# Kernel tuning notes

Hardware: AMD Instinct MI355X
Metric: run time of the kernel (lower is better)

Reference implementation:

```python
import jax, jax.numpy as jnp
import numpy as np
from jax import lax

B, TGT, SRC = 2, 1024, 1024
D_MODEL, D_INNER, D_STATE, D_CONV, DT_RANK, D_FF, N_HEADS = 1024, 2048, 16, 4, 64, 4096, 16
EPS = 1e-6


def rmsnorm(x, w):
    return x * lax.rsqrt(jnp.mean(x * x, axis=-1, keepdims=True) + EPS) * w


def weight_quant(w):
    # BitNet b1.58 ternary weight quantization (absmean), straight-through
    s = jnp.clip(jnp.mean(jnp.abs(w)), 1e-5, None)
    wq = jnp.clip(jnp.round(w / s), -1.0, 1.0) * s
    return w + lax.stop_gradient(wq - w)


def act_quant(x):
    # per-token 8-bit absmax activation quantization, straight-through
    s = jnp.clip(jnp.max(jnp.abs(x), axis=-1, keepdims=True), 1e-5, None) / 127.0
    xq = jnp.clip(jnp.round(x / s), -128.0, 127.0) * s
    return x + lax.stop_gradient(xq - x)


def mamba_block(x, in_w, conv_w, conv_b, xproj_w, dt_w, dt_b, A_log, D, out_w):
    # x: (b, L, d_model)
    xz = x @ in_w.T                              # (b, L, 2*d_inner)
    u, res = jnp.split(xz, 2, axis=-1)
    # causal depthwise conv over sequence
    uc = lax.conv_general_dilated(
        u.transpose(0, 2, 1), conv_w, (1,), [(D_CONV - 1, 0)],
        dimension_numbers=('NCH', 'OIH', 'NCH'), feature_group_count=D_INNER)
    u = jax.nn.silu((uc + conv_b[None, :, None]).transpose(0, 2, 1))  # (b, L, d_inner)
    proj = u @ xproj_w.T                         # (b, L, dt_rank + 2*d_state)
    dt, Bm, Cm = jnp.split(proj, [DT_RANK, DT_RANK + D_STATE], axis=-1)
    delta = jax.nn.softplus(dt @ dt_w.T + dt_b)  # (b, L, d_inner)
    A = -jnp.exp(A_log)                          # (d_inner, d_state)
    dA = jnp.exp(delta[..., None] * A)                       # (b, L, d_inner, d_state)
    dBu = (delta * u)[..., None] * Bm[:, :, None, :]         # (b, L, d_inner, d_state)

    def step(h, t):
        da, dbu, c = t
        h = da * h + dbu
        return h, jnp.einsum('bds,bs->bd', h, c)

    h0 = jnp.zeros((x.shape[0], D_INNER, D_STATE), x.dtype)
    _, ys = lax.scan(step, h0, (dA.transpose(1, 0, 2, 3), dBu.transpose(1, 0, 2, 3), Cm.transpose(1, 0, 2)))
    y = ys.transpose(1, 0, 2) + u * D
    return (y * jax.nn.silu(res)) @ out_w.T


def cross_attention(x, enc, mask, qw, qb, kw, kb, vw, vb, ow, ob):
    hd = D_MODEL // N_HEADS
    b, t, _ = x.shape
    s = enc.shape[1]
    q = (x @ qw.T + qb).reshape(b, t, N_HEADS, hd)
    k = (enc @ kw.T + kb).reshape(b, s, N_HEADS, hd)
    v = (enc @ vw.T + vb).reshape(b, s, N_HEADS, hd)
    sc = jnp.einsum('bthd,bshd->bhts', q, k) / np.sqrt(hd)
    sc = jnp.where(mask[:, None, None, :], sc, -1e9)
    a = jax.nn.softmax(sc, axis=-1)
    o = jnp.einsum('bhts,bshd->bthd', a, v).reshape(b, t, D_MODEL)
    return o @ ow.T + ob


def bitnet_ffn(x, w1, b1, w2, b2):
    h = jax.nn.gelu(act_quant(x) @ weight_quant(w1).T + b1)
    return act_quant(h) @ weight_quant(w2).T + b2


def setup_inputs() -> dict:
    key = jax.random.key(0)
    ks = iter(jax.random.split(key, 32))
    n = lambda shape, sc=0.02: (jax.random.normal(next(ks), shape, jnp.float32) * sc)
    inp = {
        'x': jax.random.normal(next(ks), (B, TGT, D_MODEL), jnp.float32),
        'encoder_out': jax.random.normal(next(ks), (B, SRC, D_MODEL), jnp.float32),
        'encoder_mask': jnp.ones((B, SRC), dtype=bool),
        'mamba_in_w': n((2 * D_INNER, D_MODEL)),
        'mamba_conv_w': n((D_INNER, 1, D_CONV), 0.2),
        'mamba_conv_b': jnp.zeros((D_INNER,), jnp.float32),
        'mamba_xproj_w': n((DT_RANK + 2 * D_STATE, D_INNER)),
        'mamba_dt_w': n((D_INNER, DT_RANK)),
        'mamba_dt_b': jnp.full((D_INNER,), -4.0, jnp.float32),
        'mamba_A_log': jnp.broadcast_to(jnp.log(jnp.arange(1, D_STATE + 1, dtype=jnp.float32)), (D_INNER, D_STATE)).copy(),
        'mamba_D': jnp.ones((D_INNER,), jnp.float32),
        'mamba_out_w': n((D_MODEL, D_INNER)),
        'norm1_w': jnp.ones((D_MODEL,), jnp.float32),
        'q_w': n((D_MODEL, D_MODEL)), 'q_b': jnp.zeros((D_MODEL,), jnp.float32),
        'k_w': n((D_MODEL, D_MODEL)), 'k_b': jnp.zeros((D_MODEL,), jnp.float32),
        'v_w': n((D_MODEL, D_MODEL)), 'v_b': jnp.zeros((D_MODEL,), jnp.float32),
        'o_w': n((D_MODEL, D_MODEL)), 'o_b': jnp.zeros((D_MODEL,), jnp.float32),
        'norm2_w': jnp.ones((D_MODEL,), jnp.float32),
        'ffn_w1': n((D_FF, D_MODEL)), 'ffn_b1': jnp.zeros((D_FF,), jnp.float32),
        'ffn_w2': n((D_MODEL, D_FF)), 'ffn_b2': jnp.zeros((D_MODEL,), jnp.float32),
        'norm3_w': jnp.ones((D_MODEL,), jnp.float32),
    }
    return inp


def reference(x, encoder_out, encoder_mask, mamba_in_w, mamba_conv_w, mamba_conv_b,
              mamba_xproj_w, mamba_dt_w, mamba_dt_b, mamba_A_log, mamba_D, mamba_out_w,
              norm1_w, q_w, q_b, k_w, k_b, v_w, v_b, o_w, o_b, norm2_w,
              ffn_w1, ffn_b1, ffn_w2, ffn_b2, norm3_w):
    residual = x
    h = mamba_block(x, mamba_in_w, mamba_conv_w, mamba_conv_b, mamba_xproj_w,
                    mamba_dt_w, mamba_dt_b, mamba_A_log, mamba_D, mamba_out_w)
    h = rmsnorm(residual + h, norm1_w)  # dropout = identity (eval)
    residual = h
    a = cross_attention(h, encoder_out, encoder_mask, q_w, q_b, k_w, k_b, v_w, v_b, o_w, o_b)
    h = rmsnorm(residual + a, norm2_w)
    residual = h
    f = bitnet_ffn(h, ffn_w1, ffn_b1, ffn_w2, ffn_b2)
    return rmsnorm(residual + f, norm3_w)
```

## Files before the change

kernel.cpp:

```cpp
#include <hip/hip_runtime.h>
#include <math.h>

#define DEV __device__ __forceinline__
using u16 = unsigned short;
typedef __bf16 bh8 __attribute__((ext_vector_type(8)));
typedef float f32x4 __attribute__((ext_vector_type(4)));
typedef u16 u16x8 __attribute__((ext_vector_type(8)));
typedef u16 u16x4 __attribute__((ext_vector_type(4)));

DEV float b2f(u16 x){ unsigned u = ((unsigned)x) << 16; float f; __builtin_memcpy(&f, &u, 4); return f; }
DEV u16 f2b(float f){ unsigned u; __builtin_memcpy(&u, &f, 4); return (u16)((u + 0x7fffu + ((u >> 16) & 1u)) >> 16); }
DEV float sigm(float x){ return 1.f / (1.f + __expf(-x)); }
DEV float ldf(const void* p, size_t i, bool f32){ return f32 ? ((const float*)p)[i] : b2f(((const u16*)p)[i]); }

__global__ __launch_bounds__(256) void detect_kernel(const void* x, unsigned* flag)
{
  const int tid = threadIdx.x;
  const u16* p = (const u16*)x;
  int sane = 0;
  #pragma unroll
  for (int j = 0; j < 8; j++){
    u16 v = p[(size_t)(tid * 8 + j) * 2];
    int e = (v >> 7) & 0xFF;
    sane += (e >= 0x60 && e <= 0x8F) ? 1 : 0;
  }
  __shared__ int red[256];
  red[tid] = sane; __syncthreads();
  for (int s = 128; s > 0; s >>= 1){ if (tid < s) red[tid] += red[tid + s]; __syncthreads(); }
  if (tid == 0) flag[0] = (red[0] < 1200) ? 1u : 0u;
}

#define NCVT 17
struct CvtJobs {
  const void* src[NCVT];
  u16* dst[NCVT];
  int n[NCVT];
  int blk_off[NCVT + 1];
};
__global__ __launch_bounds__(256) void convert_kernel(CvtJobs jobs, const unsigned* __restrict__ Fg)
{
  const bool f32 = Fg[0] != 0;
  const int bx = blockIdx.x;
  int j = 0;
  while (bx >= jobs.blk_off[j + 1]) j++;
  const int e = (bx - jobs.blk_off[j]) * 2048 + threadIdx.x * 8;
  if (e >= jobs.n[j]) return;
  if (f32){
    const float* s = (const float*)jobs.src[j] + e;
    u16x8 o;
    #pragma unroll
    for (int i = 0; i < 8; i++) o[i] = f2b(s[i]);
    *(u16x8*)(jobs.dst[j] + e) = o;
  } else {
    *(u16x8*)(jobs.dst[j] + e) = *(const u16x8*)((const u16*)jobs.src[j] + e);
  }
}

template<int EPI, int FM, int FN, int WR, int WC>
__global__ __launch_bounds__(256) void gemm16(
    const u16* __restrict__ A, const u16* __restrict__ W, void* __restrict__ Cv,
    int M, int N, int K, int lda, int ldb, int ldc,
    const u16* __restrict__ bias, const float* __restrict__ rowscale,
    const float* __restrict__ wscale)
{
  constexpr int BM = WR * FM * 16, BN = WC * FN * 16;
  __shared__ __align__(16) char As[BM * 128];
  __shared__ __align__(16) char Bs[BN * 128];
  const int tid = threadIdx.x, wave = tid >> 6, lane = tid & 63;
  const int wr = wave / WC, wc = wave % WC, fr = lane & 15, g = lane >> 4;
  const size_t bm = (size_t)blockIdx.y * BM, bn = (size_t)blockIdx.x * BN;
  const int kbase = blockIdx.z * K;
  f32x4 acc[FM][FN] = {};
  constexpr int ACH = BM / 32, BCH = BN / 32;
  u16x8 areg[ACH], breg[BCH];
  auto fetch = [&](int k0){
    #pragma unroll
    for (int c = 0; c < ACH; c++){
      int li = tid + c * 256;
      areg[c] = *(const u16x8*)&A[(bm + (li >> 3)) * (size_t)lda + kbase + k0 + ((li & 7) << 3)];
    }
    #pragma unroll
    for (int c = 0; c < BCH; c++){
      int li = tid + c * 256;
      breg[c] = *(const u16x8*)&W[(bn + (li >> 3)) * (size_t)ldb + kbase + k0 + ((li & 7) << 3)];
    }
  };
  fetch(0);
  for (int k0 = 0; k0 < K; k0 += 64){
    __syncthreads();
    #pragma unroll
    for (int c = 0; c < ACH; c++){
      int li = tid + c * 256, row = li >> 3, j = li & 7;
      *(u16x8*)&As[row * 128 + ((j * 16) ^ ((row & 7) << 4))] = areg[c];
    }
    #pragma unroll
    for (int c = 0; c < BCH; c++){
      int li = tid + c * 256, row = li >> 3, j = li & 7;
      *(u16x8*)&Bs[row * 128 + ((j * 16) ^ ((row & 7) << 4))] = breg[c];
    }
    __syncthreads();
    if (k0 + 64 < K) fetch(k0 + 64);
    bh8 af[2][FM], bf[2][FN];
    #pragma unroll
    for (int ks = 0; ks < 2; ks++){
      #pragma unroll
      for (int i = 0; i < FM; i++){
        int row = wr * (FM * 16) + i * 16 + fr;
        af[ks][i] = *(const bh8*)&As[row * 128 + ((ks * 64 + g * 16) ^ ((row & 7) << 4))];
      }
      #pragma unroll
      for (int j = 0; j < FN; j++){
        int row = wc * (FN * 16) + j * 16 + fr;
        bf[ks][j] = *(const bh8*)&Bs[row * 128 + ((ks * 64 + g * 16) ^ ((row & 7) << 4))];
      }
    }
    #pragma unroll
    for (int ks = 0; ks < 2; ks++)
      #pragma unroll
      for (int i = 0; i < FM; i++)
        #pragma unroll
        for (int j = 0; j < FN; j++)
          acc[i][j] = __builtin_amdgcn_mfma_f32_16x16x32_bf16(af[ks][i], bf[ks][j], acc[i][j], 0, 0, 0);
  }
  float wsc = 0.f;
  if constexpr (EPI == 4 || EPI == 5) wsc = wscale[0];
  u16* Cb = (u16*)Cv;
  float* Cf = (float*)Cv + (size_t)blockIdx.z * M * ldc;
  #pragma unroll
  for (int i = 0; i < FM; i++){
    #pragma unroll
    for (int r = 0; r < 4; r++){
      const size_t row = bm + wr * (FM * 16) + i * 16 + g * 4 + r;
      float rs = 0.f;
      if constexpr (EPI == 4 || EPI == 5) rs = rowscale[row] * wsc;
      #pragma unroll
      for (int j = 0; j < FN; j++){
        const size_t col = bn + wc * (FN * 16) + j * 16 + fr;
        float v = acc[i][j][r];
        if constexpr (EPI == 1 || EPI == 2) v += b2f(bias[col]);
        if constexpr (EPI == 4 || EPI == 5) v = v * rs + b2f(bias[col]);
        if constexpr (EPI == 4){ float x = v; v = 0.5f * x * (1.f + tanhf(0.7978845608f * (x + 0.044715f * x * x * x))); }
        if constexpr (EPI == 6){ float x = v + b2f(bias[col]); v = fmaxf(x, 0.f) + log1pf(__expf(-fabsf(x))); }
        if constexpr (EPI == 0 || EPI == 1 || EPI == 4) Cb[row * ldc + col] = f2b(v);
        else Cf[row * ldc + col] = v;
      }
    }
  }
}

__global__ __launch_bounds__(256) void xproj_reduce_kernel(
    const float* __restrict__ Pp, float* __restrict__ proj, u16* __restrict__ projb)
{
  const int idx = blockIdx.x * 256 + threadIdx.x;
  const int m = idx / 96, n = idx % 96;
  float s = 0.f;
  #pragma unroll
  for (int z = 0; z < 8; z++) s += Pp[(size_t)z * 2048 * 96 + idx];
  proj[idx] = s;
  if (n < 64) projb[(size_t)m * 64 + n] = f2b(s);
}

__global__ __launch_bounds__(256) void conv_silu_kernel(
    const u16* __restrict__ xz, const void* __restrict__ cw, const void* __restrict__ cb,
    u16* __restrict__ u, const unsigned* __restrict__ Fg)
{
  const bool f32 = Fg[0] != 0;
  const int idx = blockIdx.x * 256 + threadIdx.x;
  const int c = idx & 2047;
  const int bt = idx >> 11;
  const int t = bt & 1023, b = bt >> 10;
  float acc = ldf(cb, c, f32);
  #pragma unroll
  for (int j = 0; j < 4; j++){
    int tt = t - 3 + j;
    if (tt >= 0) acc += b2f(xz[(size_t)(b * 1024 + tt) * 4096 + c]) * ldf(cw, c * 4 + j, f32);
  }
  u[(size_t)bt * 2048 + c] = f2b(acc * sigm(acc));
}

#define SCH 32
#define SNCH 32

__global__ __launch_bounds__(256) void scan_part1(
    const float* __restrict__ delta, const u16* __restrict__ u,
    const float* __restrict__ proj, const void* __restrict__ Alog,
    float* __restrict__ S, float* __restrict__ sumdl_o, const unsigned* __restrict__ Fg)
{
  const bool f32 = Fg[0] != 0;
  const int b = blockIdx.z, ch = blockIdx.y, d = blockIdx.x * 256 + threadIdx.x;
  float A[16], h[16];
  #pragma unroll
  for (int s = 0; s < 16; s++){ A[s] = -__expf(ldf(Alog, d * 16 + s, f32)); h[s] = 0.f; }
  __shared__ __align__(16) float Bsh[SCH][16];
  {
    int tc = threadIdx.x >> 3, j = (threadIdx.x & 7) * 2;
    *(float2*)&Bsh[tc][j] = *(const float2*)&proj[(size_t)(b * 1024 + ch * SCH + tc) * 96 + 64 + j];
  }
  __syncthreads();
  float sumdl = 0.f;
  for (int tt = 0; tt < SCH; tt++){
    const size_t m = (size_t)(b * 1024 + ch * SCH + tt);
    const float dl = delta[m * 2048 + d];
    const float du = dl * b2f(u[m * 2048 + d]);
    sumdl += dl;
    #pragma unroll
    for (int s = 0; s < 16; s++) h[s] = __expf(dl * A[s]) * h[s] + du * Bsh[tt][s];
  }
  #pragma unroll
  for (int s = 0; s < 16; s++) S[((size_t)(b * SNCH + ch) * 16 + s) * 2048 + d] = h[s];
  sumdl_o[(size_t)(b * SNCH + ch) * 2048 + d] = sumdl;
}

__global__ __launch_bounds__(256) void scan_combine(
    const float* __restrict__ S, const float* __restrict__ sumdl,
    const void* __restrict__ Alog, float* __restrict__ Hin, const unsigned* __restrict__ Fg)
{
  const bool f32 = Fg[0] != 0;
  const int idx = blockIdx.x * 256 + threadIdx.x;
  const int b = idx >> 11, d = idx & 2047;
  float A[16], h[16];
  #pragma unroll
  for (int s = 0; s < 16; s++){ A[s] = -__expf(ldf(Alog, d * 16 + s, f32)); h[s] = 0.f; }
  for (int ch = 0; ch < SNCH; ch++){
    const float sd = sumdl[(size_t)(b * SNCH + ch) * 2048 + d];
    #pragma unroll
    for (int s = 0; s < 16; s++){
      const size_t off = ((size_t)(b * SNCH + ch) * 16 + s) * 2048 + d;
      Hin[off] = h[s];
      h[s] = __expf(A[s] * sd) * h[s] + S[off];
    }
  }
}

__global__ __launch_bounds__(256) void scan_part2(
    const float* __restrict__ delta, const u16* __restrict__ u,
    const float* __restrict__ proj, const void* __restrict__ Alog,
    const void* __restrict__ Dp, const u16* __restrict__ xz,
    const float* __restrict__ Hin, u16* __restrict__ G, const unsigned* __restrict__ Fg)
{
  const bool f32 = Fg[0] != 0;
  const int b = blockIdx.z, ch = blockIdx.y, d = blockIdx.x * 256 + threadIdx.x;
  float A[16], h[16];
  #pragma unroll
  for (int s = 0; s < 16; s++){
    A[s] = -__expf(ldf(Alog, d * 16 + s, f32));
    h[s] = Hin[((size_t)(b * SNCH + ch) * 16 + s) * 2048 + d];
  }
  const float Dv = ldf(Dp, d, f32);
  __shared__ __align__(16) float BCs[SCH][32];
  {
    int tc = threadIdx.x >> 3, j = (threadIdx.x & 7) * 4;
    *(float4*)&BCs[tc][j] = *(const float4*)&proj[(size_t)(b * 1024 + ch * SCH + tc) * 96 + 64 + j];
  }
  __syncthreads();
  for (int tt = 0; tt < SCH; tt++){
    const size_t m = (size_t)(b * 1024 + ch * SCH + tt);
    const float dl = delta[m * 2048 + d];
    const float uv = b2f(u[m * 2048 + d]);
    const float du = dl * uv;
    float y = 0.f;
    #pragma unroll
    for (int s = 0; s < 16; s++){
      h[s] = __expf(dl * A[s]) * h[s] + du * BCs[tt][s];
      y += h[s] * BCs[tt][16 + s];
    }
    y += uv * Dv;
    const float r = b2f(xz[m * 4096 + 2048 + d]);
    G[m * 2048 + d] = f2b(y * (r * sigm(r)));
  }
}

__global__ __launch_bounds__(256) void vtrans_kernel(const u16* __restrict__ V, u16* __restrict__ Vt)
{
  __shared__ __align__(16) u16 T[64 * 64];
  const int bh = blockIdx.y, b = bh >> 4, hh = bh & 15;
  const int s0 = blockIdx.x * 64;
  const int tid = threadIdx.x;
  {
    int s = tid & 63, d0 = (tid >> 6) * 16;
    const u16* src = V + ((size_t)(b * 1024 + s0 + s)) * 1024 + hh * 64 + d0;
    u16x8 v0 = *(const u16x8*)src, v1 = *(const u16x8*)(src + 8);
    int byte0 = (s * 128 + d0 * 2) ^ ((s & 7) << 4);
    int byte1 = (s * 128 + d0 * 2 + 16) ^ ((s & 7) << 4);
    *(u16x8*)((char*)T + byte0) = v0;
    *(u16x8*)((char*)T + byte1) = v1;
  }
  __syncthreads();
  {
    int d = tid & 63, t0 = (tid >> 6) * 16;
    u16x8 w0, w1;
    #pragma unroll
    for (int j = 0; j < 8; j++){
      int r0 = t0 + j, r1 = t0 + 8 + j;
      w0[j] = *(const u16*)((char*)T + ((r0 * 128 + d * 2) ^ ((r0 & 7) << 4)));
      w1[j] = *(const u16*)((char*)T + ((r1 * 128 + d * 2) ^ ((r1 & 7) << 4)));
    }
    u16* dst = Vt + ((size_t)bh * 64 + d) * 1024 + s0 + t0;
    *(u16x8*)dst = w0;
    *(u16x8*)(dst + 8) = w1;
  }
}

#define ASPL 4
__global__ __launch_bounds__(64) void attn_split_kernel(
    const u16* __restrict__ Q, const u16* __restrict__ Kb, const u16* __restrict__ Vt,
    u16* __restrict__ Opart, float* __restrict__ Lpart)
{
  const int bh = blockIdx.y, b = bh >> 4, hh = bh & 15;
  const int q0 = blockIdx.x * 16, z = blockIdx.z;
  const int lane = threadIdx.x, fr = lane & 15, g = lane >> 4;
  __shared__ __align__(16) u16 Pl[1024];
  const u16* qp = Q + ((size_t)(b * 1024 + q0 + fr)) * 1024 + hh * 64 + g * 8;
  const bh8 aq0 = *(const bh8*)qp;
  const bh8 aq1 = *(const bh8*)(qp + 32);
  f32x4 oacc[4] = {};
  float lsum[4] = {};
  const u16* kbase = Kb + ((size_t)(b * 1024)) * 1024 + hh * 64;
  const u16* vbase = Vt + ((size_t)bh * 64) * 1024;
  for (int s0 = z * (1024 / ASPL); s0 < (z + 1) * (1024 / ASPL); s0 += 64){
    bh8 bk[4][2], bv[2][4];
    #pragma unroll
    for (int ct = 0; ct < 4; ct++)
      #pragma unroll
      for (int ks = 0; ks < 2; ks++)
        bk[ct][ks] = *(const bh8*)(kbase + (size_t)(s0 + 16 * ct + fr) * 1024 + ks * 32 + g * 8);
    #pragma unroll
    for (int ks = 0; ks < 2; ks++)
      #pragma unroll
      for (int dt = 0; dt < 4; dt++)
        bv[ks][dt] = *(const bh8*)(vbase + (size_t)(16 * dt + fr) * 1024 + s0 + ks * 32 + g * 8);
    #pragma unroll
    for (int ct = 0; ct < 4; ct++){
      f32x4 zz = {};
      zz = __builtin_amdgcn_mfma_f32_16x16x32_bf16(aq0, bk[ct][0], zz, 0, 0, 0);
      zz = __builtin_amdgcn_mfma_f32_16x16x32_bf16(aq1, bk[ct][1], zz, 0, 0, 0);
      #pragma unroll
      for (int r = 0; r < 4; r++){
        float p = __expf(zz[r] * 0.125f);
        u16 pb = f2b(p);
        lsum[r] += b2f(pb);
        int row = 4 * g + r, col = 16 * ct + fr;
        *(u16*)((char*)Pl + ((row * 128 + col * 2) ^ ((row & 7) << 4))) = pb;
      }
    }
    bh8 pa[2];
    #pragma unroll
    for (int ks = 0; ks < 2; ks++)
      pa[ks] = *(const bh8*)((char*)Pl + ((fr * 128 + (ks * 32 + g * 8) * 2) ^ ((fr & 7) << 4)));
    #pragma unroll
    for (int dt = 0; dt < 4; dt++){
      oacc[dt] = __builtin_amdgcn_mfma_f32_16x16x32_bf16(pa[0], bv[0][dt], oacc[dt], 0, 0, 0);
      oacc[dt] = __builtin_amdgcn_mfma_f32_16x16x32_bf16(pa[1], bv[1][dt], oacc[dt], 0, 0, 0);
    }
  }
  #pragma unroll
  for (int r = 0; r < 4; r++){
    #pragma unroll
    for (int d2 = 1; d2 < 16; d2 <<= 1) lsum[r] += __shfl_xor(lsum[r], d2);
  }
  u16* opz = Opart + (size_t)z * 2097152;
  #pragma unroll
  for (int r = 0; r < 4; r++){
    const int tok = b * 1024 + q0 + 4 * g + r;
    #pragma unroll
    for (int dt = 0; dt < 4; dt++)
      opz[(size_t)tok * 1024 + hh * 64 + 16 * dt + fr] = f2b(oacc[dt][r]);
    if (fr == 0) Lpart[(size_t)z * 32768 + tok * 16 + hh] = lsum[r];
  }
}

__global__ __launch_bounds__(256) void attn_combine_kernel(
    const u16* __restrict__ Opart, const float* __restrict__ Lpart, u16* __restrict__ O)
{
  const int tok = blockIdx.x, tid = threadIdx.x;
  const int c = tid * 4, hh = c >> 6;
  float l = 0.f;
  #pragma unroll
  for (int z = 0; z < ASPL; z++) l += Lpart[(size_t)z * 32768 + tok * 16 + hh];
  float acc[4] = {};
  #pragma unroll
  for (int z = 0; z < ASPL; z++){
    u16x4 v = *(const u16x4*)&Opart[(size_t)z * 2097152 + (size_t)tok * 1024 + c];
    #pragma unroll
    for (int j = 0; j < 4; j++) acc[j] += b2f(v[j]);
  }
  const float inv = 1.f / l;
  u16x4 ov;
  #pragma unroll
  for (int j = 0; j < 4; j++) ov[j] = f2b(acc[j] * inv);
  *(u16x4*)&O[(size_t)tok * 1024 + c] = ov;
}

__global__ __launch_bounds__(256) void rmsnorm_kernel(
    const void* __restrict__ a, int aIn, const float* __restrict__ bsrc,
    const void* __restrict__ w, u16* __restrict__ outb, float* __restrict__ outf,
    void* __restrict__ dout, const unsigned* __restrict__ Fg)
{
  const bool f32 = Fg[0] != 0;
  const bool a32 = aIn ? f32 : true;
  const int row = blockIdx.x, tid = threadIdx.x;
  const size_t base = (size_t)row * 1024 + tid * 4;
  float v[4];
  if (a32){
    float4 t = *(const float4*)&((const float*)a)[base];
    v[0] = t.x; v[1] = t.y; v[2] = t.z; v[3] = t.w;
  } else {
    u16x4 t = *(const u16x4*)&((const u16*)a)[base];
    v[0] = b2f(t[0]); v[1] = b2f(t[1]); v[2] = b2f(t[2]); v[3] = b2f(t[3]);
  }
  float4 t2 = *(const float4*)&bsrc[base];
  v[0] += t2.x; v[1] += t2.y; v[2] += t2.z; v[3] += t2.w;
  float ss = v[0]*v[0] + v[1]*v[1] + v[2]*v[2] + v[3]*v[3];
  __shared__ float red[256];
  red[tid] = ss; __syncthreads();
  for (int s = 128; s > 0; s >>= 1){ if (tid < s) red[tid] += red[tid + s]; __syncthreads(); }
  const float scale = rsqrtf(red[0] * (1.f / 1024.f) + 1e-6f);
  float o[4];
  #pragma unroll
  for (int i = 0; i < 4; i++) o[i] = v[i] * scale * ldf(w, tid * 4 + i, f32);
  if (outb){
    u16x4 ov;
    #pragma unroll
    for (int i = 0; i < 4; i++) ov[i] = f2b(o[i]);
    *(u16x4*)&outb[base] = ov;
  }
  if (outf) *(float4*)&outf[base] = make_float4(o[0], o[1], o[2], o[3]);
  if (dout){
    if (f32) ((float*)dout)[base] = o[0], ((float*)dout)[base+1] = o[1], ((float*)dout)[base+2] = o[2], ((float*)dout)[base+3] = o[3];
    else {
      u16x4 ov;
      #pragma unroll
      for (int i = 0; i < 4; i++) ov[i] = f2b(o[i]);
      *(u16x4*)&((u16*)dout)[base] = ov;
    }
  }
}

__global__ __launch_bounds__(256) void actquant_kernel(
    const void* __restrict__ in, int inF32, u16* __restrict__ q, float* __restrict__ srow, int N)
{
  const int row = blockIdx.x, tid = threadIdx.x;
  float amax = 0.f;
  for (int c = tid * 4; c < N; c += 1024){
    #pragma unroll
    for (int j = 0; j < 4; j++){
      float x = inF32 ? ((const float*)in)[(size_t)row * N + c + j] : b2f(((const u16*)in)[(size_t)row * N + c + j]);
      amax = fmaxf(amax, fabsf(x));
    }
  }
  __shared__ float red[256];
  red[tid] = amax; __syncthreads();
  for (int s = 128; s > 0; s >>= 1){ if (tid < s) red[tid] = fmaxf(red[tid], red[tid + s]); __syncthreads(); }
  const float s = fmaxf(red[0], 1e-5f) * (1.f / 127.f);
  if (tid == 0) srow[row] = s;
  for (int c = tid * 4; c < N; c += 1024){
    u16x4 ov;
    #pragma unroll
    for (int j = 0; j < 4; j++){
      float x = inF32 ? ((const float*)in)[(size_t)row * N + c + j] : b2f(((const u16*)in)[(size_t)row * N + c + j]);
      ov[j] = f2b(fminf(fmaxf(rintf(x / s), -128.f), 127.f));
    }
    *(u16x4*)&q[(size_t)row * N + c] = ov;
  }
}

__global__ __launch_bounds__(256) void absmean_partial_kernel(
    const void* __restrict__ w, float* __restrict__ part, const unsigned* __restrict__ Fg)
{
  const bool f32 = Fg[0] != 0;
  const int tid = threadIdx.x;
  const size_t base = (size_t)blockIdx.x * 1024 + tid * 4;
  float ssum = 0.f;
  #pragma unroll
  for (int j = 0; j < 4; j++) ssum += fabsf(ldf(w, base + j, f32));
  __shared__ float red[256];
  red[tid] = ssum; __syncthreads();
  for (int s = 128; s > 0; s >>= 1){ if (tid < s) red[tid] += red[tid + s]; __syncthreads(); }
  if (tid == 0) part[blockIdx.x] = red[0];
}

__global__ __launch_bounds__(256) void absmean_final_kernel(
    const float* __restrict__ part, int n, float invc, float* __restrict__ out)
{
  const int tid = threadIdx.x;
  float ssum = 0.f;
  for (int i = tid; i < n; i += 256) ssum += part[i];
  __shared__ float red[256];
  red[tid] = ssum; __syncthreads();
  for (int s = 128; s > 0; s >>= 1){ if (tid < s) red[tid] += red[tid + s]; __syncthreads(); }
  if (tid == 0) out[0] = fmaxf(red[0] * invc, 1e-5f);
}

__global__ __launch_bounds__(256) void ternarize_kernel(
    const void* __restrict__ w, const float* __restrict__ sp, u16* __restrict__ t,
    const unsigned* __restrict__ Fg)
{
  const bool f32 = Fg[0] != 0;
  const float s = sp[0];
  const size_t base = ((size_t)blockIdx.x * 256 + threadIdx.x) * 4;
  u16x4 o;
  #pragma unroll
  for (int i = 0; i < 4; i++){
    float vv = fminf(fmaxf(rintf(ldf(w, base + i, f32) / s), -1.f), 1.f);
    o[i] = f2b(vv);
  }
  *(u16x4*)&t[base] = o;
}

extern "C" void kernel_launch(void* const* d_in, const int* in_sizes, int n_in,
                              void* d_out, int out_size, void* d_ws, size_t ws_size,
                              hipStream_t stream)
{
  const void* x      = d_in[0];
  const void* enc    = d_in[1];
  const void* in_w   = d_in[3];
  const void* conv_w = d_in[4];
  const void* conv_b = d_in[5];
  const void* xproj_w= d_in[6];
  const void* dt_w   = d_in[7];
  const void* dt_b   = d_in[8];
  const void* A_log  = d_in[9];
  const void* Dp     = d_in[10];
  const void* out_w  = d_in[11];
  const void* n1w    = d_in[12];
  const void* q_w = d_in[13]; const void* q_b = d_in[14];
  const void* k_w = d_in[15]; const void* k_b = d_in[16];
  const void* v_w = d_in[17]; const void* v_b = d_in[18];
  const void* o_w = d_in[19]; const void* o_b = d_in[20];
  const void* n2w = d_in[21];
  const void* w1  = d_in[22]; const void* b1 = d_in[23];
  const void* w2  = d_in[24]; const void* b2 = d_in[25];
  const void* n3w = d_in[26];

  char* ws = (char*)d_ws;
  const size_t MB = 1ull << 20;
  const size_t KB = 1024;
  float*    sw1  = (float*)(ws + 0);
  float*    sw2  = (float*)(ws + 16);
  unsigned* Fg   = (unsigned*)(ws + 64);
  float*    s1   = (float*)(ws + 4096);
  float*    s2   = (float*)(ws + 12288);
  float*    part = (float*)(ws + 20480);
  u16*   xz   = (u16*)  (ws + 1 * MB);
  u16*   u    = (u16*)  (ws + 17 * MB);
  float* proj = (float*)(ws + 25 * MB);
  float* delta= (float*)(ws + 26 * MB);
  float* Pp   = (float*)(ws + 42 * MB);
  u16*   projb= (u16*)  (ws + 48 * MB);
  u16*   G    = (u16*)  (ws + 42 * MB);
  float* Ssc  = (float*)(ws + 50 * MB);
  float* Hin  = (float*)(ws + 58 * MB);
  float* sdl  = (float*)(ws + 66 * MB);
  float* mout = (float*)(ws + 50 * MB);
  u16*   h1b  = (u16*)  (ws + 26 * MB);
  float* h1f  = (float*)(ws + 30 * MB);
  u16*   qb   = (u16*)  (ws + 1 * MB);
  u16*   kb   = (u16*)  (ws + 5 * MB);
  u16*   vb   = (u16*)  (ws + 9 * MB);
  u16*   vtb  = (u16*)  (ws + 38 * MB);
  u16*   Opart= (u16*)  (ws + 42 * MB);
  float* Lpart= (float*)(ws + 66 * MB);
  u16*   ao   = (u16*)  (ws + 13 * MB);
  float* aof  = (float*)(ws + 17 * MB);
  float* h2f  = (float*)(ws + 58 * MB);
  u16*   q1   = (u16*)  (ws + 1 * MB);
  u16*   t1   = (u16*)  (ws + 5 * MB);
  u16*   t2   = (u16*)  (ws + 50 * MB);
  u16*   gh   = (u16*)  (ws + 13 * MB);
  u16*   q2   = (u16*)  (ws + 29 * MB);
  float* fo   = (float*)(ws + 1 * MB);
  u16* xb       = (u16*)(ws + 68 * MB);
  u16* encb     = (u16*)(ws + 72 * MB);
  u16* in_wb    = (u16*)(ws + 76 * MB);
  u16* out_wb   = (u16*)(ws + 84 * MB);
  u16* q_wb     = (u16*)(ws + 88 * MB);
  u16* k_wb     = (u16*)(ws + 90 * MB);
  u16* v_wb     = (u16*)(ws + 92 * MB);
  u16* o_wb     = (u16*)(ws + 94 * MB);
  u16* xproj_wb = (u16*)(ws + 96 * MB);
  u16* dt_wb    = (u16*)(ws + 96 * MB + 512 * KB);
  u16* dt_bb    = (u16*)(ws + 96 * MB + 768 * KB);
  u16* q_bb     = (u16*)(ws + 96 * MB + 776 * KB);
  u16* k_bb     = (u16*)(ws + 96 * MB + 780 * KB);
  u16* v_bb     = (u16*)(ws + 96 * MB + 784 * KB);
  u16* o_bb     = (u16*)(ws + 96 * MB + 788 * KB);
  u16* b1b      = (u16*)(ws + 96 * MB + 792 * KB);
  u16* b2b      = (u16*)(ws + 96 * MB + 808 * KB);

  dim3 blk(256);
  detect_kernel<<<dim3(1), blk, 0, stream>>>(x, Fg);

  {
    CvtJobs jobs;
    const void* srcs[NCVT] = { x, enc, in_w, out_w, q_w, k_w, v_w, o_w, xproj_w, dt_w,
                               dt_b, q_b, k_b, v_b, o_b, b1, b2 };
    u16* dsts[NCVT] = { xb, encb, in_wb, out_wb, q_wb, k_wb, v_wb, o_wb, xproj_wb, dt_wb,
                        dt_bb, q_bb, k_bb, v_bb, o_bb, b1b, b2b };
    int ns[NCVT] = { 2097152, 2097152, 4194304, 2097152, 1048576, 1048576, 1048576, 1048576,
                     196608, 131072, 2048, 1024, 1024, 1024, 1024, 4096, 1024 };
    int bo = 0;
    for (int j = 0; j < NCVT; j++){
      jobs.src[j] = srcs[j]; jobs.dst[j] = dsts[j]; jobs.n[j] = ns[j];
      jobs.blk_off[j] = bo;
      bo += (ns[j] / 8 + 255) / 256;
    }
    jobs.blk_off[NCVT] = bo;
    convert_kernel<<<dim3(bo), blk, 0, stream>>>(jobs, Fg);
  }

  gemm16<0,4,4,2,2><<<dim3(32, 16), blk, 0, stream>>>(xb, in_wb, xz, 2048, 4096, 1024, 1024, 1024, 4096, nullptr, nullptr, nullptr);
  conv_silu_kernel<<<dim3(16384), blk, 0, stream>>>(xz, conv_w, conv_b, u, Fg);
  gemm16<3,2,3,2,2><<<dim3(1, 32, 8), blk, 0, stream>>>(u, xproj_wb, Pp, 2048, 96, 256, 2048, 2048, 96, nullptr, nullptr, nullptr);
  xproj_reduce_kernel<<<dim3(768), blk, 0, stream>>>(Pp, proj, projb);
  gemm16<6,2,2,2,2><<<dim3(32, 32), blk, 0, stream>>>(projb, dt_wb, delta, 2048, 2048, 64, 64, 64, 2048, dt_bb, nullptr, nullptr);
  scan_part1<<<dim3(8, SNCH, 2), blk, 0, stream>>>(delta, u, proj, A_log, Ssc, sdl, Fg);
  scan_combine<<<dim3(16), blk, 0, stream>>>(Ssc, sdl, A_log, Hin, Fg);
  scan_part2<<<dim3(8, SNCH, 2), blk, 0, stream>>>(delta, u, proj, A_log, Dp, xz, Hin, G, Fg);
  gemm16<3,2,2,2,2><<<dim3(16, 32), blk, 0, stream>>>(G, out_wb, mout, 2048, 1024, 2048, 2048, 2048, 1024, nullptr, nullptr, nullptr);
  rmsnorm_kernel<<<dim3(2048), blk, 0, stream>>>(x, 1, mout, n1w, h1b, h1f, nullptr, Fg);
  gemm16<1,2,2,2,2><<<dim3(16, 32), blk, 0, stream>>>(h1b, q_wb, qb, 2048, 1024, 1024, 1024, 1024, 1024, q_bb, nullptr, nullptr);
  gemm16<1,2,2,2,2><<<dim3(16, 32), blk, 0, stream>>>(encb, k_wb, kb, 2048, 1024, 1024, 1024, 1024, 1024, k_bb, nullptr, nullptr);
  gemm16<1,2,2,2,2><<<dim3(16, 32), blk, 0, stream>>>(encb, v_wb, vb, 2048, 1024, 1024, 1024, 1024, 1024, v_bb, nullptr, nullptr);
  vtrans_kernel<<<dim3(16, 32), blk, 0, stream>>>(vb, vtb);
  attn_split_kernel<<<dim3(64, 32, ASPL), dim3(64), 0, stream>>>(qb, kb, vtb, Opart, Lpart);
  attn_combine_kernel<<<dim3(2048), blk, 0, stream>>>(Opart, Lpart, ao);
  gemm16<2,2,2,2,2><<<dim3(16, 32), blk, 0, stream>>>(ao, o_wb, aof, 2048, 1024, 1024, 1024, 1024, 1024, o_bb, nullptr, nullptr);
  rmsnorm_kernel<<<dim3(2048), blk, 0, stream>>>(h1f, 0, aof, n2w, nullptr, h2f, nullptr, Fg);
  actquant_kernel<<<dim3(2048), blk, 0, stream>>>(h2f, 1, q1, s1, 1024);
  absmean_partial_kernel<<<dim3(4096), blk, 0, stream>>>(w1, part, Fg);
  absmean_final_kernel<<<dim3(1), blk, 0, stream>>>(part, 4096, 1.f / 4194304.f, sw1);
  ternarize_kernel<<<dim3(4096), blk, 0, stream>>>(w1, sw1, t1, Fg);
  absmean_partial_kernel<<<dim3(4096), blk, 0, stream>>>(w2, part, Fg);
  absmean_final_kernel<<<dim3(1), blk, 0, stream>>>(part, 4096, 1.f / 4194304.f, sw2);
  ternarize_kernel<<<dim3(4096), blk, 0, stream>>>(w2, sw2, t2, Fg);
  gemm16<4,4,4,2,2><<<dim3(32, 16), blk, 0, stream>>>(q1, t1, gh, 2048, 4096, 1024, 1024, 1024, 4096, b1b, s1, sw1);
  actquant_kernel<<<dim3(2048), blk, 0, stream>>>(gh, 0, q2, s2, 4096);
  gemm16<5,2,2,2,2><<<dim3(16, 32), blk, 0, stream>>>(q2, t2, fo, 2048, 1024, 4096, 4096, 4096, 1024, b2b, s2, sw2);
  rmsnorm_kernel<<<dim3(2048), blk, 0, stream>>>(h2f, 0, fo, n3w, nullptr, nullptr, d_out, Fg);
}
```

Measured before the change: 457.3 us.

## Share K/V tiles across four waves in LDS for cross-attention

Replaces the single-wave attention kernel with a 256-thread kernel in which four waves, each handling 16 queries, cooperatively stage the 64-key K and V^T tiles into swizzled shared memory and read their MFMA operands from there. This cuts redundant global/L2 loads of K and V, which were previously fetched independently by every 16-query wave. The key-dimension split is also halved from 4 to 2, which reduces partial outputs and combine work but means fewer blocks and longer per-block loops. Two block-wide barriers are added per key tile.

```diff
diff --git a/kernel.cpp b/kernel.cpp
--- a/kernel.cpp
+++ b/kernel.cpp
@@ -301,15 +301,19 @@
   }
 }
 
-#define ASPL 4
-__global__ __launch_bounds__(64) void attn_split_kernel(
+#define ASPL 2
+__global__ __launch_bounds__(256) void attn_mw_kernel(
     const u16* __restrict__ Q, const u16* __restrict__ Kb, const u16* __restrict__ Vt,
     u16* __restrict__ Opart, float* __restrict__ Lpart)
 {
   const int bh = blockIdx.y, b = bh >> 4, hh = bh & 15;
-  const int q0 = blockIdx.x * 16, z = blockIdx.z;
-  const int lane = threadIdx.x, fr = lane & 15, g = lane >> 4;
-  __shared__ __align__(16) u16 Pl[1024];
+  const int z = blockIdx.z;
+  const int tid = threadIdx.x, wave = tid >> 6, lane = tid & 63;
+  const int fr = lane & 15, g = lane >> 4;
+  const int q0 = blockIdx.x * 64 + wave * 16;
+  __shared__ __align__(16) char Ks[64 * 128];
+  __shared__ __align__(16) char Vs[64 * 128];
+  __shared__ __align__(16) u16 Pl[4][1024];
   const u16* qp = Q + ((size_t)(b * 1024 + q0 + fr)) * 1024 + hh * 64 + g * 8;
   const bh8 aq0 = *(const bh8*)qp;
   const bh8 aq1 = *(const bh8*)(qp + 32);
@@ -317,18 +321,35 @@
   float lsum[4] = {};
   const u16* kbase = Kb + ((size_t)(b * 1024)) * 1024 + hh * 64;
   const u16* vbase = Vt + ((size_t)bh * 64) * 1024;
+  const int srow = tid >> 2, sj = (tid & 3) * 2;
   for (int s0 = z * (1024 / ASPL); s0 < (z + 1) * (1024 / ASPL); s0 += 64){
+    __syncthreads();
+    {
+      const u16* kr = kbase + (size_t)(s0 + srow) * 1024 + sj * 8;
+      u16x8 k0 = *(const u16x8*)kr, k1 = *(const u16x8*)(kr + 8);
+      *(u16x8*)&Ks[srow * 128 + ((sj * 16) ^ ((srow & 7) << 4))] = k0;
+      *(u16x8*)&Ks[srow * 128 + (((sj + 1) * 16) ^ ((srow & 7) << 4))] = k1;
+      const u16* vr = vbase + (size_t)srow * 1024 + s0 + sj * 8;
+      u16x8 v0 = *(const u16x8*)vr, v1 = *(const u16x8*)(vr + 8);
+      *(u16x8*)&Vs[srow * 128 + ((sj * 16) ^ ((srow & 7) << 4))] = v0;
+      *(u16x8*)&Vs[srow * 128 + (((sj + 1) * 16) ^ ((srow & 7) << 4))] = v1;
+    }
+    __syncthreads();
     bh8 bk[4][2], bv[2][4];
     #pragma unroll
-    for (int ct = 0; ct < 4; ct++)
+    for (int ct = 0; ct < 4; ct++){
+      int row = 16 * ct + fr;
       #pragma unroll
       for (int ks = 0; ks < 2; ks++)
-        bk[ct][ks] = *(const bh8*)(kbase + (size_t)(s0 + 16 * ct + fr) * 1024 + ks * 32 + g * 8);
-    #pragma unroll
-    for (int ks = 0; ks < 2; ks++)
-      #pragma unroll
-      for (int dt = 0; dt < 4; dt++)
-        bv[ks][dt] = *(const bh8*)(vbase + (size_t)(16 * dt + fr) * 1024 + s0 + ks * 32 + g * 8);
+        bk[ct][ks] = *(const bh8*)&Ks[row * 128 + ((ks * 64 + g * 16) ^ ((row & 7) << 4))];
+    }
+    #pragma unroll
+    for (int dt = 0; dt < 4; dt++){
+      int row = 16 * dt + fr;
+      #pragma unroll
+      for (int ks = 0; ks < 2; ks++)
+        bv[ks][dt] = *(const bh8*)&Vs[row * 128 + ((ks * 64 + g * 16) ^ ((row & 7) << 4))];
+    }
     #pragma unroll
     for (int ct = 0; ct < 4; ct++){
       f32x4 zz = {};
@@ -340,13 +361,13 @@
         u16 pb = f2b(p);
         lsum[r] += b2f(pb);
         int row = 4 * g + r, col = 16 * ct + fr;
-        *(u16*)((char*)Pl + ((row * 128 + col * 2) ^ ((row & 7) << 4))) = pb;
+        *(u16*)((char*)&Pl[wave][0] + ((row * 128 + col * 2) ^ ((row & 7) << 4))) = pb;
       }
     }
     bh8 pa[2];
     #pragma unroll
     for (int ks = 0; ks < 2; ks++)
-      pa[ks] = *(const bh8*)((char*)Pl + ((fr * 128 + (ks * 32 + g * 8) * 2) ^ ((fr & 7) << 4)));
+      pa[ks] = *(const bh8*)((char*)&Pl[wave][0] + ((fr * 128 + (ks * 32 + g * 8) * 2) ^ ((fr & 7) << 4)));
     #pragma unroll
     for (int dt = 0; dt < 4; dt++){
       oacc[dt] = __builtin_amdgcn_mfma_f32_16x16x32_bf16(pa[0], bv[0][dt], oacc[dt], 0, 0, 0);
@@ -622,7 +643,7 @@
   gemm16<1,2,2,2,2><<<dim3(16, 32), blk, 0, stream>>>(encb, k_wb, kb, 2048, 1024, 1024, 1024, 1024, 1024, k_bb, nullptr, nullptr);
   gemm16<1,2,2,2,2><<<dim3(16, 32), blk, 0, stream>>>(encb, v_wb, vb, 2048, 1024, 1024, 1024, 1024, 1024, v_bb, nullptr, nullptr);
   vtrans_kernel<<<dim3(16, 32), blk, 0, stream>>>(vb, vtb);
-  attn_split_kernel<<<dim3(64, 32, ASPL), dim3(64), 0, stream>>>(qb, kb, vtb, Opart, Lpart);
+  attn_mw_kernel<<<dim3(16, 32, ASPL), blk, 0, stream>>>(qb, kb, vtb, Opart, Lpart);
   attn_combine_kernel<<<dim3(2048), blk, 0, stream>>>(Opart, Lpart, ao);
   gemm16<2,2,2,2,2><<<dim3(16, 32), blk, 0, stream>>>(ao, o_wb, aof, 2048, 1024, 1024, 1024, 1024, 1024, o_bb, nullptr, nullptr);
   rmsnorm_kernel<<<dim3(2048), blk, 0, stream>>>(h1f, 0, aof, n2w, nullptr, h2f, nullptr, Fg);
```

New measurement: 415.3 us. 1.1x faster.
